# Performance work log

Hardware: AMD Instinct MI355X
Metric: run time of the kernel (lower is better)

The kernel has to match this reference:

```python
import jax, jax.numpy as jnp
import numpy as np

DIM = 768
HEADS = 12
HEAD_DIM = DIM // HEADS
SEQ = 196
BATCH = 64
SCALE = HEAD_DIM ** -0.5


def setup_inputs() -> dict:
    key = jax.random.key(0)
    ks = jax.random.split(key, 5)
    x = jax.random.normal(ks[0], (BATCH, SEQ, DIM), dtype=jnp.float32)
    W_qkv = jax.random.normal(ks[1], (DIM, 3 * DIM), dtype=jnp.float32) * (DIM ** -0.5)
    static_a = jax.random.truncated_normal(ks[2], -2.0, 2.0, (1, HEADS, SEQ, SEQ), dtype=jnp.float32)
    W_proj = jax.random.normal(ks[3], (DIM, DIM), dtype=jnp.float32) * (DIM ** -0.5)
    b_proj = jnp.zeros((DIM,), dtype=jnp.float32)
    return {"x": x, "W_qkv": W_qkv, "static_a": static_a, "W_proj": W_proj, "b_proj": b_proj}


def reference(x, W_qkv, static_a, W_proj, b_proj):
    B, N, C = x.shape
    qkv = (x @ W_qkv).reshape(B, N, 3, HEADS, HEAD_DIM)
    qkv = jnp.transpose(qkv, (2, 0, 3, 1, 4))  # [3, B, H, N, D]
    q, k, v = qkv[0], qkv[1], qkv[2]
    attn = jnp.einsum('bhnd,bhmd->bhnm', q, k) * SCALE
    attn = jax.nn.softmax(attn, axis=-1) + static_a  # post-softmax additive bias
    out = jnp.einsum('bhnm,bhmd->bhnd', attn, v)  # [B, H, N, D]
    out = jnp.transpose(out, (0, 2, 1, 3)).reshape(B, N, C)
    return out @ W_proj + b_proj
```

## Files before the change

kernel.cpp:

```cpp
#include <hip/hip_runtime.h>
#include <stdint.h>

#define DIM 768
#define HEADS 12
#define SEQ 196
#define BATCH 64
#define NTOK (BATCH*SEQ)
#define SCALE 0.125f

using short8  = __attribute__((ext_vector_type(8))) short;
using float4v = __attribute__((ext_vector_type(4))) float;
using ushort4v = __attribute__((ext_vector_type(4))) unsigned short;

static __device__ __forceinline__ unsigned short f2bf(float f) {
  union { float f; unsigned u; } v; v.f = f;
  unsigned u = v.u;
  u += 0x7fffu + ((u >> 16) & 1u);
  return (unsigned short)(u >> 16);
}

#if defined(__has_builtin)
#if __has_builtin(__builtin_amdgcn_global_load_lds)
#define HAS_GLL 1
#endif
#endif

static __device__ __forceinline__ void gll16(const unsigned short* g, unsigned short* l) {
#ifdef HAS_GLL
  __builtin_amdgcn_global_load_lds(
      (const __attribute__((address_space(1))) void*)g,
      (__attribute__((address_space(3))) void*)l, 16, 0, 0);
#else
  const int lane = threadIdx.x & 63;
  *(short8*)(l + lane * 8) = *(const short8*)g;
#endif
}

__global__ __launch_bounds__(256) void cast_x_kernel(const float* __restrict__ in,
                                                     unsigned short* __restrict__ out) {
  int i = blockIdx.x * 256 + threadIdx.x;
  float4 v = ((const float4*)in)[i];
  ushort4v o;
  o.x = f2bf(v.x); o.y = f2bf(v.y); o.z = f2bf(v.z); o.w = f2bf(v.w);
  ((ushort4v*)out)[i] = o;
}

__global__ __launch_bounds__(256) void transpose_cast_kernel(const float* __restrict__ in,
                                                             unsigned short* __restrict__ out,
                                                             int R, int C) {
  __shared__ float tile[32][33];
  int c0 = blockIdx.x * 32, r0 = blockIdx.y * 32;
  int tx = threadIdx.x, ty = threadIdx.y;
  for (int i = 0; i < 32; i += 8)
    tile[ty + i][tx] = in[(size_t)(r0 + ty + i) * C + c0 + tx];
  __syncthreads();
  for (int i = 0; i < 32; i += 8)
    out[(size_t)(c0 + ty + i) * R + r0 + tx] = f2bf(tile[tx][ty + i]);
}

template <int MODE>
__global__ __launch_bounds__(256) void gemm_kernel(const unsigned short* __restrict__ A,
                                                   const unsigned short* __restrict__ Bt,
                                                   const float* __restrict__ bias,
                                                   unsigned short* __restrict__ outQKV,
                                                   float* __restrict__ outF) {
  constexpr int K = 768;
  __shared__ __align__(16) unsigned short Als[128 * 32];
  __shared__ __align__(16) unsigned short Bls[128 * 32];
  const int tid = threadIdx.x;
  const int wid = tid >> 6, lane = tid & 63;
  const int s = lane & 15, q = lane >> 4;
  const int wr = wid >> 1, wc = wid & 1;
  const int m0 = blockIdx.y * 128;
  const int n0 = blockIdx.x * 128;

  float4v acc[4][4];
  for (int i = 0; i < 4; i++)
    for (int j = 0; j < 4; j++) acc[i][j] = (float4v){0.f, 0.f, 0.f, 0.f};

  const int srow = lane >> 2;
  const int scol = (lane & 3) * 8;

  for (int kt = 0; kt < K; kt += 32) {
    const unsigned short* ga = A  + (size_t)(m0 + wid * 32 + srow) * K + kt + scol;
    const unsigned short* gb = Bt + (size_t)(n0 + wid * 32 + srow) * K + kt + scol;
    unsigned short* la = &Als[wid * 32 * 32];
    unsigned short* lb = &Bls[wid * 32 * 32];
    gll16(ga,           la);
    gll16(ga + 16 * K,  la + 16 * 32);
    gll16(gb,           lb);
    gll16(gb + 16 * K,  lb + 16 * 32);
    __syncthreads();

    short8 af[4], bf[4];
    for (int i = 0; i < 4; i++)
      af[i] = *(const short8*)&Als[(wr * 64 + i * 16 + s) * 32 + q * 8];
    for (int j = 0; j < 4; j++)
      bf[j] = *(const short8*)&Bls[(wc * 64 + j * 16 + s) * 32 + q * 8];
    for (int i = 0; i < 4; i++)
      for (int j = 0; j < 4; j++)
        acc[i][j] = __builtin_amdgcn_mfma_f32_16x16x32_bf16(af[i], bf[j], acc[i][j], 0, 0, 0);
    __syncthreads();
  }

  for (int i = 0; i < 4; i++) {
    int mbase = m0 + wr * 64 + i * 16 + q * 4;
    for (int j = 0; j < 4; j++) {
      int ng = n0 + wc * 64 + j * 16 + s;
      if (MODE == 0) {
        int t = ng / 768, rem = ng % 768;
        int h = rem >> 6, d = rem & 63;
        for (int r = 0; r < 4; r++) {
          int mg = mbase + r;
          int b = mg / 196, ns = mg - b * 196;
          size_t off = ((size_t)((t * BATCH + b) * HEADS + h) * SEQ + ns) * 64 + d;
          outQKV[off] = f2bf(acc[i][j][r]);
        }
      } else {
        float bv = bias[ng];
        for (int r = 0; r < 4; r++)
          outF[(size_t)(mbase + r) * 768 + ng] = acc[i][j][r] + bv;
      }
    }
  }
}

__global__ __launch_bounds__(256) void attn_kernel(const unsigned short* __restrict__ qkv,
                                                   const float* __restrict__ static_a,
                                                   unsigned short* __restrict__ outA) {
  constexpr int WV = 232;
  __shared__ __align__(16) unsigned short Vt[64 * WV];
  __shared__ __align__(16) unsigned short Aw[4 * 16 * WV];
  const int tid = threadIdx.x, wid = tid >> 6, lane = tid & 63;
  const int s = lane & 15, q = lane >> 4;
  const int bh = blockIdx.x;
  const int b = bh / 12, h = bh % 12;
  const size_t slab = (size_t)SEQ * 64;
  const unsigned short* Qb = qkv + (size_t)(0 * BATCH * HEADS + bh) * slab;
  const unsigned short* Kb = qkv + (size_t)(1 * BATCH * HEADS + bh) * slab;
  const unsigned short* Vb = qkv + (size_t)(2 * BATCH * HEADS + bh) * slab;

  for (int idx = tid; idx < SEQ * 16; idx += 256) {
    int m = idx >> 4;
    int d4 = (idx & 15) * 4;
    ushort4v v = *(const ushort4v*)&Vb[m * 64 + d4];
    Vt[(d4 + 0) * WV + m] = v.x; Vt[(d4 + 1) * WV + m] = v.y;
    Vt[(d4 + 2) * WV + m] = v.z; Vt[(d4 + 3) * WV + m] = v.w;
  }
  for (int idx = tid; idx < 64 * 28; idx += 256) {
    int d = idx / 28, m = 196 + idx % 28;
    Vt[d * WV + m] = 0;
  }
  __syncthreads();

  for (int qt = wid; qt < 13; qt += 4) {
    int n0 = qt * 16;
    int qrow = n0 + s; if (qrow > 195) qrow = 195;
    short8 qf0 = *(const short8*)&Qb[qrow * 64 + q * 8];
    short8 qf1 = *(const short8*)&Qb[qrow * 64 + 32 + q * 8];

    float4v sacc[13];
    for (int mt = 0; mt < 13; mt++) {
      int mrow = mt * 16 + s; if (mrow > 195) mrow = 195;
      short8 kf0 = *(const short8*)&Kb[mrow * 64 + q * 8];
      short8 kf1 = *(const short8*)&Kb[mrow * 64 + 32 + q * 8];
      float4v z = (float4v){0.f, 0.f, 0.f, 0.f};
      z = __builtin_amdgcn_mfma_f32_16x16x32_bf16(qf0, kf0, z, 0, 0, 0);
      z = __builtin_amdgcn_mfma_f32_16x16x32_bf16(qf1, kf1, z, 0, 0, 0);
      sacc[mt] = z;
    }

    bool lastvalid = (s < 4);
    float mx[4], sm[4];
    for (int i = 0; i < 4; i++) mx[i] = -3.0e38f;
    for (int mt = 0; mt < 13; mt++) {
      bool v = (mt < 12) || lastvalid;
      if (v)
        for (int i = 0; i < 4; i++) mx[i] = fmaxf(mx[i], sacc[mt][i] * SCALE);
    }
    for (int off = 1; off < 16; off <<= 1)
      for (int i = 0; i < 4; i++) mx[i] = fmaxf(mx[i], __shfl_xor(mx[i], off, 16));
    for (int i = 0; i < 4; i++) sm[i] = 0.f;
    for (int mt = 0; mt < 13; mt++) {
      bool v = (mt < 12) || lastvalid;
      for (int i = 0; i < 4; i++) {
        float e = v ? __expf(sacc[mt][i] * SCALE - mx[i]) : 0.f;
        sacc[mt][i] = e;
        sm[i] += e;
      }
    }
    for (int off = 1; off < 16; off <<= 1)
      for (int i = 0; i < 4; i++) sm[i] += __shfl_xor(sm[i], off, 16);
    float inv[4];
    for (int i = 0; i < 4; i++) inv[i] = 1.0f / sm[i];

    unsigned short* Arow = &Aw[wid * 16 * WV];
    for (int mt = 0; mt < 13; mt++) {
      bool v = (mt < 12) || lastvalid;
      int m = mt * 16 + s;
      for (int i = 0; i < 4; i++) {
        int n = n0 + q * 4 + i; int ncl = n > 195 ? 195 : n;
        float a = 0.f;
        if (v) a = sacc[mt][i] * inv[i] + static_a[(h * SEQ + ncl) * SEQ + m];
        Arow[(q * 4 + i) * WV + m] = f2bf(a);
      }
    }
    {
      int m = 208 + s;
      for (int i = 0; i < 4; i++) Arow[(q * 4 + i) * WV + m] = 0;
    }
    asm volatile("s_waitcnt lgkmcnt(0)" ::: "memory");

    short8 af[7];
    for (int ks = 0; ks < 7; ks++)
      af[ks] = *(const short8*)&Arow[s * WV + ks * 32 + q * 8];
    for (int dt = 0; dt < 4; dt++) {
      float4v o = (float4v){0.f, 0.f, 0.f, 0.f};
      for (int ks = 0; ks < 7; ks++) {
        short8 vf = *(const short8*)&Vt[(dt * 16 + s) * WV + ks * 32 + q * 8];
        o = __builtin_amdgcn_mfma_f32_16x16x32_bf16(af[ks], vf, o, 0, 0, 0);
      }
      for (int i = 0; i < 4; i++) {
        int ng = n0 + q * 4 + i;
        if (ng < 196) {
          size_t off = ((size_t)(b * SEQ + ng) * DIM) + h * 64 + dt * 16 + s;
          outA[off] = f2bf(o[i]);
        }
      }
    }
  }
}

extern "C" void kernel_launch(void* const* d_in, const int* in_sizes, int n_in,
                              void* d_out, int out_size, void* d_ws, size_t ws_size,
                              hipStream_t stream) {
  const float* x        = (const float*)d_in[0];
  const float* Wqkv     = (const float*)d_in[1];
  const float* static_a = (const float*)d_in[2];
  const float* Wproj    = (const float*)d_in[3];
  const float* bproj    = (const float*)d_in[4];
  float* out = (float*)d_out;

  unsigned char* ws = (unsigned char*)d_ws;
  size_t off = 0;
  unsigned short* qkv_ws = (unsigned short*)(ws + off); off += (size_t)3 * NTOK * DIM * 2;
  unsigned short* xa_ws  = (unsigned short*)(ws + off); off += (size_t)NTOK * DIM * 2;
  unsigned short* wqkvt  = (unsigned short*)(ws + off); off += (size_t)3 * DIM * DIM * 2;
  unsigned short* wprojt = (unsigned short*)(ws + off); off += (size_t)DIM * DIM * 2;

  cast_x_kernel<<<NTOK * DIM / 4 / 256, 256, 0, stream>>>(x, xa_ws);
  transpose_cast_kernel<<<dim3(3 * DIM / 32, DIM / 32), dim3(32, 8), 0, stream>>>(Wqkv, wqkvt, DIM, 3 * DIM);
  transpose_cast_kernel<<<dim3(DIM / 32, DIM / 32), dim3(32, 8), 0, stream>>>(Wproj, wprojt, DIM, DIM);
  gemm_kernel<0><<<dim3(3 * DIM / 128, NTOK / 128), 256, 0, stream>>>(xa_ws, wqkvt, nullptr, qkv_ws, nullptr);
  attn_kernel<<<BATCH * HEADS, 256, 0, stream>>>(qkv_ws, static_a, xa_ws);
  gemm_kernel<1><<<dim3(DIM / 128, NTOK / 128), 256, 0, stream>>>(xa_ws, wprojt, bproj, nullptr, out);
}
```

Baseline: 265.8 us.

## Keep softmax probabilities in registers via transposed MFMA and permuted key order

The attention kernel now computes S transposed (K as the A operand), with key rows permuted so that each lane's accumulator values map directly onto the B-operand fragment of the P·V MFMA. This removes the per-wave LDS staging buffer for the probability matrix and its write/read round trip. The row max and sum reductions now need only two cross-lane shuffles instead of four per row. The exp uses exp2 with a folded scale, static_a is read as float4 vectors, and output is written as 4-wide vector stores. The V transpose staging is reworked with a 228-element row stride and 16-element chunks per thread. The risks are more LDS bank conflicts from the new stride and split 64-bit V reads, plus higher register pressure from holding the probability fragments in registers.

```diff
diff --git a/kernel.cpp b/kernel.cpp
--- a/kernel.cpp
+++ b/kernel.cpp
@@ -9,6 +9,7 @@
 #define SCALE 0.125f
 
 using short8  = __attribute__((ext_vector_type(8))) short;
+using short4v = __attribute__((ext_vector_type(4))) short;
 using float4v = __attribute__((ext_vector_type(4))) float;
 using ushort4v = __attribute__((ext_vector_type(4))) unsigned short;
 
@@ -128,9 +129,8 @@
 __global__ __launch_bounds__(256) void attn_kernel(const unsigned short* __restrict__ qkv,
                                                    const float* __restrict__ static_a,
                                                    unsigned short* __restrict__ outA) {
-  constexpr int WV = 232;
+  constexpr int WV = 228;
   __shared__ __align__(16) unsigned short Vt[64 * WV];
-  __shared__ __align__(16) unsigned short Aw[4 * 16 * WV];
   const int tid = threadIdx.x, wid = tid >> 6, lane = tid & 63;
   const int s = lane & 15, q = lane >> 4;
   const int bh = blockIdx.x;
@@ -140,92 +140,107 @@
   const unsigned short* Kb = qkv + (size_t)(1 * BATCH * HEADS + bh) * slab;
   const unsigned short* Vb = qkv + (size_t)(2 * BATCH * HEADS + bh) * slab;
 
-  for (int idx = tid; idx < SEQ * 16; idx += 256) {
-    int m = idx >> 4;
-    int d4 = (idx & 15) * 4;
-    ushort4v v = *(const ushort4v*)&Vb[m * 64 + d4];
-    Vt[(d4 + 0) * WV + m] = v.x; Vt[(d4 + 1) * WV + m] = v.y;
-    Vt[(d4 + 2) * WV + m] = v.z; Vt[(d4 + 3) * WV + m] = v.w;
-  }
-  for (int idx = tid; idx < 64 * 28; idx += 256) {
-    int d = idx / 28, m = 196 + idx % 28;
-    Vt[d * WV + m] = 0;
+  {
+    const int ms = tid & 63;
+    const int d0 = (tid >> 6) * 16;
+    for (int mb = 0; mb < 4; ++mb) {
+      int m = mb * 64 + ms;
+      if (m < 224) {
+        if (m < 196) {
+          short8 v0 = *(const short8*)&Vb[(size_t)m * 64 + d0];
+          short8 v1 = *(const short8*)&Vb[(size_t)m * 64 + d0 + 8];
+          for (int j = 0; j < 8; j++) Vt[(d0 + j) * WV + m] = (unsigned short)v0[j];
+          for (int j = 0; j < 8; j++) Vt[(d0 + 8 + j) * WV + m] = (unsigned short)v1[j];
+        } else {
+          for (int j = 0; j < 16; j++) Vt[(d0 + j) * WV + m] = 0;
+        }
+      }
+    }
   }
   __syncthreads();
 
+  const int pmbase = (s >> 2) * 8 + (s & 3);
+
   for (int qt = wid; qt < 13; qt += 4) {
-    int n0 = qt * 16;
-    int qrow = n0 + s; if (qrow > 195) qrow = 195;
-    short8 qf0 = *(const short8*)&Qb[qrow * 64 + q * 8];
-    short8 qf1 = *(const short8*)&Qb[qrow * 64 + 32 + q * 8];
-
-    float4v sacc[13];
-    for (int mt = 0; mt < 13; mt++) {
-      int mrow = mt * 16 + s; if (mrow > 195) mrow = 195;
-      short8 kf0 = *(const short8*)&Kb[mrow * 64 + q * 8];
-      short8 kf1 = *(const short8*)&Kb[mrow * 64 + 32 + q * 8];
+    const int n0 = qt * 16;
+    const int nq = n0 + s;
+    const int nql = nq > 195 ? 195 : nq;
+    short8 qf0 = *(const short8*)&Qb[(size_t)nql * 64 + q * 8];
+    short8 qf1 = *(const short8*)&Qb[(size_t)nql * 64 + 32 + q * 8];
+
+    float4v sacc[14];
+    for (int tt = 0; tt < 13; tt++) {
+      int t = tt >> 1, h4 = tt & 1;
+      int m = t * 32 + h4 * 4 + pmbase;
+      if (m > 195) m = 195;
+      short8 kf0 = *(const short8*)&Kb[(size_t)m * 64 + q * 8];
+      short8 kf1 = *(const short8*)&Kb[(size_t)m * 64 + 32 + q * 8];
       float4v z = (float4v){0.f, 0.f, 0.f, 0.f};
-      z = __builtin_amdgcn_mfma_f32_16x16x32_bf16(qf0, kf0, z, 0, 0, 0);
-      z = __builtin_amdgcn_mfma_f32_16x16x32_bf16(qf1, kf1, z, 0, 0, 0);
-      sacc[mt] = z;
-    }
-
-    bool lastvalid = (s < 4);
-    float mx[4], sm[4];
-    for (int i = 0; i < 4; i++) mx[i] = -3.0e38f;
-    for (int mt = 0; mt < 13; mt++) {
-      bool v = (mt < 12) || lastvalid;
-      if (v)
-        for (int i = 0; i < 4; i++) mx[i] = fmaxf(mx[i], sacc[mt][i] * SCALE);
-    }
-    for (int off = 1; off < 16; off <<= 1)
-      for (int i = 0; i < 4; i++) mx[i] = fmaxf(mx[i], __shfl_xor(mx[i], off, 16));
-    for (int i = 0; i < 4; i++) sm[i] = 0.f;
-    for (int mt = 0; mt < 13; mt++) {
-      bool v = (mt < 12) || lastvalid;
+      z = __builtin_amdgcn_mfma_f32_16x16x32_bf16(kf0, qf0, z, 0, 0, 0);
+      z = __builtin_amdgcn_mfma_f32_16x16x32_bf16(kf1, qf1, z, 0, 0, 0);
+      sacc[tt] = z;
+    }
+    sacc[13] = (float4v){0.f, 0.f, 0.f, 0.f};
+
+    float mx = -3.0e38f;
+    for (int tt = 0; tt < 12; tt++)
+      for (int i = 0; i < 4; i++) mx = fmaxf(mx, sacc[tt][i]);
+    if (q == 0)
+      for (int i = 0; i < 4; i++) mx = fmaxf(mx, sacc[12][i]);
+    mx = fmaxf(mx, __shfl_xor(mx, 16));
+    mx = fmaxf(mx, __shfl_xor(mx, 32));
+    const float CE = SCALE * 1.44269504f;
+    float sm = 0.f;
+    for (int tt = 0; tt < 12; tt++)
       for (int i = 0; i < 4; i++) {
-        float e = v ? __expf(sacc[mt][i] * SCALE - mx[i]) : 0.f;
-        sacc[mt][i] = e;
-        sm[i] += e;
-      }
-    }
-    for (int off = 1; off < 16; off <<= 1)
-      for (int i = 0; i < 4; i++) sm[i] += __shfl_xor(sm[i], off, 16);
-    float inv[4];
-    for (int i = 0; i < 4; i++) inv[i] = 1.0f / sm[i];
-
-    unsigned short* Arow = &Aw[wid * 16 * WV];
-    for (int mt = 0; mt < 13; mt++) {
-      bool v = (mt < 12) || lastvalid;
-      int m = mt * 16 + s;
+        float e = __builtin_amdgcn_exp2f((sacc[tt][i] - mx) * CE);
+        sacc[tt][i] = e; sm += e;
+      }
+    if (q == 0) {
       for (int i = 0; i < 4; i++) {
-        int n = n0 + q * 4 + i; int ncl = n > 195 ? 195 : n;
-        float a = 0.f;
-        if (v) a = sacc[mt][i] * inv[i] + static_a[(h * SEQ + ncl) * SEQ + m];
-        Arow[(q * 4 + i) * WV + m] = f2bf(a);
-      }
-    }
-    {
-      int m = 208 + s;
-      for (int i = 0; i < 4; i++) Arow[(q * 4 + i) * WV + m] = 0;
-    }
-    asm volatile("s_waitcnt lgkmcnt(0)" ::: "memory");
-
-    short8 af[7];
-    for (int ks = 0; ks < 7; ks++)
-      af[ks] = *(const short8*)&Arow[s * WV + ks * 32 + q * 8];
+        float e = __builtin_amdgcn_exp2f((sacc[12][i] - mx) * CE);
+        sacc[12][i] = e; sm += e;
+      }
+    } else {
+      sacc[12] = (float4v){0.f, 0.f, 0.f, 0.f};
+    }
+    sm += __shfl_xor(sm, 16);
+    sm += __shfl_xor(sm, 32);
+    const float inv = 1.0f / sm;
+
+    const float* sa = static_a + ((size_t)h * SEQ + nql) * SEQ;
+    short8 pfrag[7];
+    for (int t = 0; t < 7; t++) {
+      short8 pf;
+      for (int h4 = 0; h4 < 2; h4++) {
+        int tt = 2 * t + h4;
+        bool valid = (tt < 12) || (tt == 12 && q == 0);
+        float4v a4 = (float4v){0.f, 0.f, 0.f, 0.f};
+        if (valid) a4 = *(const float4v*)(sa + t * 32 + q * 8 + h4 * 4);
+        int src = valid ? tt : 13;
+        for (int i = 0; i < 4; i++) {
+          float pv = valid ? (sacc[src][i] * inv + a4[i]) : 0.f;
+          pf[h4 * 4 + i] = (short)f2bf(pv);
+        }
+      }
+      pfrag[t] = pf;
+    }
+
     for (int dt = 0; dt < 4; dt++) {
       float4v o = (float4v){0.f, 0.f, 0.f, 0.f};
-      for (int ks = 0; ks < 7; ks++) {
-        short8 vf = *(const short8*)&Vt[(dt * 16 + s) * WV + ks * 32 + q * 8];
-        o = __builtin_amdgcn_mfma_f32_16x16x32_bf16(af[ks], vf, o, 0, 0, 0);
-      }
-      for (int i = 0; i < 4; i++) {
-        int ng = n0 + q * 4 + i;
-        if (ng < 196) {
-          size_t off = ((size_t)(b * SEQ + ng) * DIM) + h * 64 + dt * 16 + s;
-          outA[off] = f2bf(o[i]);
-        }
+      for (int t = 0; t < 7; t++) {
+        const unsigned short* vp = &Vt[(dt * 16 + s) * WV + t * 32 + q * 8];
+        short4v v0 = *(const short4v*)vp;
+        short4v v1 = *(const short4v*)(vp + 4);
+        short8 vf;
+        vf[0] = v0[0]; vf[1] = v0[1]; vf[2] = v0[2]; vf[3] = v0[3];
+        vf[4] = v1[0]; vf[5] = v1[1]; vf[6] = v1[2]; vf[7] = v1[3];
+        o = __builtin_amdgcn_mfma_f32_16x16x32_bf16(vf, pfrag[t], o, 0, 0, 0);
+      }
+      if (nq < 196) {
+        ushort4v ov;
+        ov.x = f2bf(o[0]); ov.y = f2bf(o[1]); ov.z = f2bf(o[2]); ov.w = f2bf(o[3]);
+        *(ushort4v*)&outA[((size_t)b * SEQ + nq) * DIM + h * 64 + dt * 16 + q * 4] = ov;
       }
     }
   }
```

After: 249.8 us. 1.06x faster.
